# Performance work log

Hardware: AMD Instinct MI355X
Metric: run time of the kernel (lower is better)

## Reference

```python
import jax, jax.numpy as jnp
import numpy as np

B, N, D, H = 4, 8192, 1024, 8
HD = D // H  # 128
EPS = 1e-5


def setup_inputs() -> dict:
    key = jax.random.key(0)
    k1, k2, k3 = jax.random.split(key, 3)
    x = jax.random.normal(k1, (B, N, D), dtype=jnp.float32)
    mask = jax.random.randint(k2, (B, 1, N), 0, 2).astype(jnp.bool_)
    # nn.Linear(dim, 3*dim, bias=False): weight [3D, D]; store as [D, 3D] for x @ w
    w_qkv = jax.random.normal(k3, (D, 3 * D), dtype=jnp.float32) / np.sqrt(D)
    gamma = jnp.ones((D,), dtype=jnp.float32)
    beta = jnp.zeros((D,), dtype=jnp.float32)
    return {"x": x, "mask": mask, "w_qkv": w_qkv, "gamma": gamma, "beta": beta}


def _layernorm(x, gamma, beta):
    mu = jnp.mean(x, axis=-1, keepdims=True)
    var = jnp.mean(jnp.square(x - mu), axis=-1, keepdims=True)
    return (x - mu) * jax.lax.rsqrt(var + EPS) * gamma + beta


def reference(x, mask, w_qkv, gamma, beta):
    xn = _layernorm(x, gamma, beta)                       # [B,N,D]
    qkv = xn @ w_qkv                                      # [B,N,3D]
    q, k, v = jnp.split(qkv, 3, axis=-1)
    # 'b n (h d) -> b h n d'
    def to_heads(t):
        return t.reshape(B, N, H, HD).transpose(0, 2, 1, 3)
    q, k, v = to_heads(q), to_heads(k), to_heads(v)       # [B,H,N,HD]
    q = jax.nn.sigmoid(q)
    k = jnp.tanh(k)
    k = jnp.where(mask[..., None], 0.0, k)                # masked_fill -> 0
    kv = jnp.einsum('bhnd,bhne->bhde', k, v)              # k^T @ v, [B,H,HD,HD]
    out = jnp.einsum('bhnd,bhde->bhne', q, kv)            # [B,H,N,HD]
    out = out.transpose(0, 2, 1, 3).reshape(B, N, D)      # 'b h n d -> b n (h d)'
    return out  # output_layer='None' -> Identity
```

## Files before the change

kernel.cpp:

```cpp
#include <hip/hip_runtime.h>

#define EPS 1e-5f
#define B_ 4
#define N_ 8192
#define D_ 1024
#define H_ 8
#define HD_ 128
#define M_TOT 32768
#define NQKV 3072

typedef __bf16 bf16x8 __attribute__((ext_vector_type(8)));
typedef float f32x4 __attribute__((ext_vector_type(4)));

__device__ __forceinline__ float bf2f(unsigned short u) {
    unsigned int v = ((unsigned int)u) << 16;
    return __uint_as_float(v);
}
__device__ __forceinline__ unsigned short f2bf(float f) {
    unsigned int u = __float_as_uint(f);
    u += 0x7fffu + ((u >> 16) & 1u);
    return (unsigned short)(u >> 16);
}

__device__ __forceinline__ float fast_sigmoid(float v) {
    return __builtin_amdgcn_rcpf(1.0f + __expf(-v));
}
__device__ __forceinline__ float fast_tanh(float v) {
    return 1.0f - 2.0f * __builtin_amdgcn_rcpf(1.0f + __expf(2.0f * v));
}

__device__ __forceinline__ void gl_lds16(const void* g, void* l) {
    __builtin_amdgcn_global_load_lds(
        (const __attribute__((address_space(1))) unsigned int*)g,
        (__attribute__((address_space(3))) unsigned int*)l, 16, 0, 0);
}

__global__ __launch_bounds__(256) void ln_kernel(const float* __restrict__ x,
                                                 const float* __restrict__ gamma,
                                                 const float* __restrict__ beta,
                                                 unsigned short* __restrict__ xn) {
    const int row = blockIdx.x;
    const int t = threadIdx.x;
    const float* xr = x + (size_t)row * D_;
    float4 xv = ((const float4*)xr)[t];
    float s = xv.x + xv.y + xv.z + xv.w;
    float s2 = xv.x * xv.x + xv.y * xv.y + xv.z * xv.z + xv.w * xv.w;
    for (int off = 32; off > 0; off >>= 1) {
        s += __shfl_down(s, off);
        s2 += __shfl_down(s2, off);
    }
    __shared__ float red[8];
    if ((t & 63) == 0) { red[t >> 6] = s; red[4 + (t >> 6)] = s2; }
    __syncthreads();
    float ts = red[0] + red[1] + red[2] + red[3];
    float ts2 = red[4] + red[5] + red[6] + red[7];
    float mu = ts * (1.0f / D_);
    float var = ts2 * (1.0f / D_) - mu * mu;
    float rs = rsqrtf(var + EPS);
    float4 g = ((const float4*)gamma)[t];
    float4 bt = ((const float4*)beta)[t];
    ushort4 o;
    o.x = f2bf((xv.x - mu) * rs * g.x + bt.x);
    o.y = f2bf((xv.y - mu) * rs * g.y + bt.y);
    o.z = f2bf((xv.z - mu) * rs * g.z + bt.z);
    o.w = f2bf((xv.w - mu) * rs * g.w + bt.w);
    ((ushort4*)(xn + (size_t)row * D_))[t] = o;
}

__global__ __launch_bounds__(256) void wt_kernel(const float* __restrict__ w,
                                                 unsigned short* __restrict__ wT) {
    __shared__ float tile[64][65];
    const int n0 = blockIdx.x * 64;
    const int k0 = blockIdx.y * 64;
    const int t = threadIdx.x;
    const int tx = t & 63, ty = t >> 6;
    #pragma unroll
    for (int i = 0; i < 16; i++) {
        int r = i * 4 + ty;
        tile[r][tx] = w[(size_t)(k0 + r) * NQKV + n0 + tx];
    }
    __syncthreads();
    #pragma unroll
    for (int i = 0; i < 16; i++) {
        int r = i * 4 + ty;
        wT[(size_t)(n0 + r) * D_ + k0 + tx] = f2bf(tile[tx][r]);
    }
}

#define CT_STRIDE 136
__global__ __launch_bounds__(256, 3) void qkv_gemm(const unsigned short* __restrict__ xn,
                                                   const unsigned short* __restrict__ wT,
                                                   const int* __restrict__ mask,
                                                   unsigned short* __restrict__ qws,
                                                   unsigned short* __restrict__ kT,
                                                   unsigned short* __restrict__ vT) {
    __shared__ unsigned short ShB[128 * CT_STRIDE];
    const int t = threadIdx.x;
    const int w = t >> 6, l = t & 63;
    const int quad = l >> 4, ln16 = l & 15;
    const int m0 = blockIdx.y * 128;
    const int n0 = blockIdx.x * 128;
    const int wm = (w >> 1) * 64, wn = (w & 1) * 64;

    f32x4 acc[4][4] = {};

    const unsigned short* aG = xn + (size_t)(m0 + w * 16 + (l >> 2)) * D_ + (l & 3) * 8;
    const unsigned short* bG = wT + (size_t)(n0 + w * 16 + (l >> 2)) * D_ + (l & 3) * 8;
    char* SB = (char*)ShB;

    for (int k0 = 0; k0 < 1024; k0 += 64) {
        #pragma unroll
        for (int s = 0; s < 2; s++) {
            gl_lds16(aG + k0 + s * 32,            SB + s * 8192 + w * 1024);
            gl_lds16(aG + 64 * D_ + k0 + s * 32,  SB + s * 8192 + 4096 + w * 1024);
            gl_lds16(bG + k0 + s * 32,            SB + 16384 + s * 8192 + w * 1024);
            gl_lds16(bG + 64 * D_ + k0 + s * 32,  SB + 16384 + s * 8192 + 4096 + w * 1024);
        }
        __syncthreads();
        #pragma unroll
        for (int s = 0; s < 2; s++) {
            const char* A0 = SB + s * 8192;
            const char* B0 = SB + 16384 + s * 8192;
            bf16x8 af[4], bfr[4];
            #pragma unroll
            for (int mi = 0; mi < 4; mi++)
                af[mi] = *(const bf16x8*)(A0 + (wm + mi * 16 + ln16) * 64 + quad * 16);
            #pragma unroll
            for (int ni = 0; ni < 4; ni++)
                bfr[ni] = *(const bf16x8*)(B0 + (wn + ni * 16 + ln16) * 64 + quad * 16);
            #pragma unroll
            for (int mi = 0; mi < 4; mi++)
                #pragma unroll
                for (int ni = 0; ni < 4; ni++)
                    acc[mi][ni] = __builtin_amdgcn_mfma_f32_16x16x32_bf16(af[mi], bfr[ni],
                                                                          acc[mi][ni], 0, 0, 0);
        }
        __syncthreads();
    }

    const int region = n0 >> 10;
    const int cbase = n0 & 1023;
    if (region == 0) {
        #pragma unroll
        for (int mi = 0; mi < 4; mi++) {
            #pragma unroll
            for (int r = 0; r < 4; r++) {
                int gm = m0 + wm + mi * 16 + quad * 4 + r;
                #pragma unroll
                for (int ni = 0; ni < 4; ni++) {
                    int cc = cbase + wn + ni * 16 + ln16;
                    qws[(size_t)gm * D_ + cc] = f2bf(fast_sigmoid(acc[mi][ni][r]));
                }
            }
        }
    } else {
        #pragma unroll
        for (int mi = 0; mi < 4; mi++) {
            int tok0 = wm + mi * 16 + quad * 4;
            int mk0 = 0, mk1 = 0, mk2 = 0, mk3 = 0;
            if (region == 1) {
                mk0 = mask[m0 + tok0];
                mk1 = mask[m0 + tok0 + 1];
                mk2 = mask[m0 + tok0 + 2];
                mk3 = mask[m0 + tok0 + 3];
            }
            #pragma unroll
            for (int ni = 0; ni < 4; ni++) {
                int fl = wn + ni * 16 + ln16;
                float v0 = acc[mi][ni][0], v1 = acc[mi][ni][1];
                float v2 = acc[mi][ni][2], v3 = acc[mi][ni][3];
                if (region == 1) {
                    v0 = mk0 ? 0.0f : fast_tanh(v0);
                    v1 = mk1 ? 0.0f : fast_tanh(v1);
                    v2 = mk2 ? 0.0f : fast_tanh(v2);
                    v3 = mk3 ? 0.0f : fast_tanh(v3);
                }
                ushort4 pk;
                pk.x = f2bf(v0); pk.y = f2bf(v1); pk.z = f2bf(v2); pk.w = f2bf(v3);
                *(ushort4*)&ShB[fl * CT_STRIDE + tok0] = pk;
            }
        }
        __syncthreads();
        unsigned short* dstT = (region == 1) ? kT : vT;
        const int h = cbase >> 7;
        const int b = m0 >> 13;
        const int ntok0 = m0 & 8191;
        #pragma unroll
        for (int p = 0; p < 8; p++) {
            int fl = p * 16 + (t >> 4);
            int tok = (t & 15) * 8;
            uint4 u = *(const uint4*)&ShB[fl * CT_STRIDE + tok];
            *(uint4*)(dstT + ((size_t)(b * 8 + h) * 128 + fl) * 8192 + ntok0 + tok) = u;
        }
    }
}

__global__ __launch_bounds__(256) void kv_mfma(const unsigned short* __restrict__ kT,
                                               const unsigned short* __restrict__ vT,
                                               float* __restrict__ kv) {
    __shared__ unsigned short As[128 * 32];
    __shared__ unsigned short Bs[128 * 32];
    const int t = threadIdx.x;
    const int w = t >> 6, l = t & 63;
    const int quad = l >> 4, ln16 = l & 15;
    const int bh = blockIdx.y;
    const int kc0 = blockIdx.x * 512;
    const int wm = (w >> 1) * 64, wn = (w & 1) * 64;

    f32x4 acc[4][4] = {};

    const size_t base = (size_t)bh * 128 * 8192;
    const unsigned short* aG = kT + base + (size_t)(w * 16 + (l >> 2)) * 8192
                               + (l & 3) * 8 + kc0;
    const unsigned short* bG = vT + base + (size_t)(w * 16 + (l >> 2)) * 8192
                               + (l & 3) * 8 + kc0;
    char* AsB = (char*)As;
    char* BsB = (char*)Bs;
    char* aL0 = AsB + w * 1024;
    char* aL1 = AsB + 4096 + w * 1024;
    char* bL0 = BsB + w * 1024;
    char* bL1 = BsB + 4096 + w * 1024;

    for (int kk = 0; kk < 512; kk += 32) {
        gl_lds16(aG + kk, aL0);
        gl_lds16(aG + 64 * 8192 + kk, aL1);
        gl_lds16(bG + kk, bL0);
        gl_lds16(bG + 64 * 8192 + kk, bL1);
        __syncthreads();
        bf16x8 af[4], bfr[4];
        #pragma unroll
        for (int mi = 0; mi < 4; mi++)
            af[mi] = *(const bf16x8*)(AsB + (wm + mi * 16 + ln16) * 64 + quad * 16);
        #pragma unroll
        for (int ni = 0; ni < 4; ni++)
            bfr[ni] = *(const bf16x8*)(BsB + (wn + ni * 16 + ln16) * 64 + quad * 16);
        #pragma unroll
        for (int mi = 0; mi < 4; mi++)
            #pragma unroll
            for (int ni = 0; ni < 4; ni++)
                acc[mi][ni] = __builtin_amdgcn_mfma_f32_16x16x32_bf16(af[mi], bfr[ni],
                                                                      acc[mi][ni], 0, 0, 0);
        __syncthreads();
    }

    float* dst = kv + (size_t)bh * (HD_ * HD_);
    #pragma unroll
    for (int mi = 0; mi < 4; mi++) {
        #pragma unroll
        for (int r = 0; r < 4; r++) {
            int d = wm + mi * 16 + quad * 4 + r;
            #pragma unroll
            for (int ni = 0; ni < 4; ni++) {
                int e = wn + ni * 16 + ln16;
                atomicAdd(&dst[d * HD_ + e], acc[mi][ni][r]);
            }
        }
    }
}

__global__ __launch_bounds__(256) void kvcvt(const float* __restrict__ kv,
                                             unsigned short* __restrict__ kvTb) {
    __shared__ float tile[32][132];
    const int bh = blockIdx.x;
    const int c = blockIdx.y;
    const int t = threadIdx.x;
    {
        int r = t >> 3, cc = (t & 7) * 16;
        const float* src = kv + ((size_t)bh * 128 + c * 32 + r) * 128 + cc;
        #pragma unroll
        for (int q4 = 0; q4 < 4; q4++)
            *(float4*)&tile[r][cc + q4 * 4] = *(const float4*)(src + q4 * 4);
    }
    __syncthreads();
    {
        int e = t >> 1, dh = t & 1;
        ushort4 o[4];
        #pragma unroll
        for (int q4 = 0; q4 < 4; q4++) {
            o[q4].x = f2bf(tile[dh * 16 + q4 * 4 + 0][e]);
            o[q4].y = f2bf(tile[dh * 16 + q4 * 4 + 1][e]);
            o[q4].z = f2bf(tile[dh * 16 + q4 * 4 + 2][e]);
            o[q4].w = f2bf(tile[dh * 16 + q4 * 4 + 3][e]);
        }
        unsigned short* dst = kvTb + (size_t)bh * 16384 + e * 128 + c * 32 + dh * 16;
        #pragma unroll
        for (int q4 = 0; q4 < 4; q4++)
            ((ushort4*)dst)[q4] = o[q4];
    }
}

__global__ __launch_bounds__(256) void out_mfma(const unsigned short* __restrict__ qws,
                                                const unsigned short* __restrict__ kvTb,
                                                float* __restrict__ out) {
    __shared__ unsigned short As[128 * 32];
    __shared__ unsigned short Bs[128 * 32];
    const int t = threadIdx.x;
    const int w = t >> 6, l = t & 63;
    const int quad = l >> 4, ln16 = l & 15;
    const int m0 = blockIdx.x * 128;
    const int h = blockIdx.y;
    const int b = m0 >> 13;
    const int bh = b * 8 + h;
    const int wm = (w >> 1) * 64, wn = (w & 1) * 64;

    f32x4 acc[4][4] = {};

    const unsigned short* aG = qws + (size_t)(m0 + w * 16 + (l >> 2)) * D_
                               + h * HD_ + (l & 3) * 8;
    const unsigned short* bG = kvTb + (size_t)bh * 16384
                               + (size_t)(w * 16 + (l >> 2)) * 128 + (l & 3) * 8;
    char* AsB = (char*)As;
    char* BsB = (char*)Bs;

    for (int kk = 0; kk < 128; kk += 32) {
        gl_lds16(aG + kk, AsB + w * 1024);
        gl_lds16(aG + 64 * D_ + kk, AsB + 4096 + w * 1024);
        gl_lds16(bG + kk, BsB + w * 1024);
        gl_lds16(bG + 64 * 128 + kk, BsB + 4096 + w * 1024);
        __syncthreads();
        bf16x8 af[4], bfr[4];
        #pragma unroll
        for (int mi = 0; mi < 4; mi++)
            af[mi] = *(const bf16x8*)(AsB + (wm + mi * 16 + ln16) * 64 + quad * 16);
        #pragma unroll
        for (int ni = 0; ni < 4; ni++)
            bfr[ni] = *(const bf16x8*)(BsB + (wn + ni * 16 + ln16) * 64 + quad * 16);
        #pragma unroll
        for (int mi = 0; mi < 4; mi++)
            #pragma unroll
            for (int ni = 0; ni < 4; ni++)
                acc[mi][ni] = __builtin_amdgcn_mfma_f32_16x16x32_bf16(af[mi], bfr[ni],
                                                                      acc[mi][ni], 0, 0, 0);
        __syncthreads();
    }

    #pragma unroll
    for (int mi = 0; mi < 4; mi++) {
        #pragma unroll
        for (int r = 0; r < 4; r++) {
            int gm = m0 + wm + mi * 16 + quad * 4 + r;
            #pragma unroll
            for (int ni = 0; ni < 4; ni++) {
                int e = wn + ni * 16 + ln16;
                out[(size_t)gm * D_ + h * HD_ + e] = acc[mi][ni][r];
            }
        }
    }
}

extern "C" void kernel_launch(void* const* d_in, const int* in_sizes, int n_in,
                              void* d_out, int out_size, void* d_ws, size_t ws_size,
                              hipStream_t stream) {
    const float* x     = (const float*)d_in[0];
    const int*   mask  = (const int*)d_in[1];
    const float* w     = (const float*)d_in[2];
    const float* gamma = (const float*)d_in[3];
    const float* beta  = (const float*)d_in[4];
    float* out = (float*)d_out;
    char* ws = (char*)d_ws;

    unsigned short* xn  = (unsigned short*)(ws + 0);
    unsigned short* wT  = (unsigned short*)(ws + 67108864ull);
    unsigned short* qws = (unsigned short*)(ws + 73400320ull);
    unsigned short* kT  = (unsigned short*)(ws + 140509184ull);
    unsigned short* vT  = (unsigned short*)(ws + 207618048ull);
    float* kv           = (float*)(ws + 274726912ull);
    unsigned short* kvTb = (unsigned short*)(ws + 276824064ull);

    hipMemsetAsync(kv, 0, 32 * HD_ * HD_ * sizeof(float), stream);
    hipLaunchKernelGGL(ln_kernel, dim3(M_TOT), dim3(256), 0, stream, x, gamma, beta, xn);
    hipLaunchKernelGGL(wt_kernel, dim3(48, 16), dim3(256), 0, stream, w, wT);
    hipLaunchKernelGGL(qkv_gemm, dim3(NQKV / 128, M_TOT / 128), dim3(256), 0, stream,
                       xn, wT, mask, qws, kT, vT);
    hipLaunchKernelGGL(kv_mfma, dim3(16, 32), dim3(256), 0, stream, kT, vT, kv);
    hipLaunchKernelGGL(kvcvt, dim3(32, 4), dim3(256), 0, stream, kv, kvTb);
    hipLaunchKernelGGL(out_mfma, dim3(M_TOT / 128, 8), dim3(256), 0, stream,
                       qws, kvTb, out);
}
```

Measured before the change: 544.6 us.

## Use one-wave LayerNorm, swizzled LDS tiles, and partial-sum KV reduction without atomics

LayerNorm now runs one 64-thread wave per row and reduces with shuffles, which drops the shared-memory reduction and its barrier. kv_mfma loads 64-wide K chunks into XOR-swizzled LDS and writes per-chunk partial KV sums to a buffer in place of float atomics. kvcvt then sums those 16 partials, which also removes the memset. out_mfma loads the full 128-wide K tile into 64 KB of swizzled LDS once, with a single barrier. The costs are more LDS per block, which may limit occupancy, and extra partial-buffer traffic; the partial buffer reuses the xn workspace region.

```diff
diff --git a/kernel.cpp b/kernel.cpp
--- a/kernel.cpp
+++ b/kernel.cpp
@@ -35,36 +35,45 @@
         (__attribute__((address_space(3))) unsigned int*)l, 16, 0, 0);
 }
 
-__global__ __launch_bounds__(256) void ln_kernel(const float* __restrict__ x,
-                                                 const float* __restrict__ gamma,
-                                                 const float* __restrict__ beta,
-                                                 unsigned short* __restrict__ xn) {
+__global__ __launch_bounds__(64) void ln_kernel(const float* __restrict__ x,
+                                                const float* __restrict__ gamma,
+                                                const float* __restrict__ beta,
+                                                unsigned short* __restrict__ xn) {
     const int row = blockIdx.x;
     const int t = threadIdx.x;
     const float* xr = x + (size_t)row * D_;
-    float4 xv = ((const float4*)xr)[t];
-    float s = xv.x + xv.y + xv.z + xv.w;
-    float s2 = xv.x * xv.x + xv.y * xv.y + xv.z * xv.z + xv.w * xv.w;
+    float4 xv[4];
+    #pragma unroll
+    for (int i = 0; i < 4; i++) xv[i] = ((const float4*)xr)[i * 64 + t];
+    float s = 0.0f, s2 = 0.0f;
+    #pragma unroll
+    for (int i = 0; i < 4; i++) {
+        s  += xv[i].x + xv[i].y + xv[i].z + xv[i].w;
+        s2 += xv[i].x * xv[i].x + xv[i].y * xv[i].y
+            + xv[i].z * xv[i].z + xv[i].w * xv[i].w;
+    }
+    #pragma unroll
     for (int off = 32; off > 0; off >>= 1) {
-        s += __shfl_down(s, off);
+        s  += __shfl_down(s, off);
         s2 += __shfl_down(s2, off);
     }
-    __shared__ float red[8];
-    if ((t & 63) == 0) { red[t >> 6] = s; red[4 + (t >> 6)] = s2; }
-    __syncthreads();
-    float ts = red[0] + red[1] + red[2] + red[3];
-    float ts2 = red[4] + red[5] + red[6] + red[7];
-    float mu = ts * (1.0f / D_);
-    float var = ts2 * (1.0f / D_) - mu * mu;
-    float rs = rsqrtf(var + EPS);
-    float4 g = ((const float4*)gamma)[t];
-    float4 bt = ((const float4*)beta)[t];
-    ushort4 o;
-    o.x = f2bf((xv.x - mu) * rs * g.x + bt.x);
-    o.y = f2bf((xv.y - mu) * rs * g.y + bt.y);
-    o.z = f2bf((xv.z - mu) * rs * g.z + bt.z);
-    o.w = f2bf((xv.w - mu) * rs * g.w + bt.w);
-    ((ushort4*)(xn + (size_t)row * D_))[t] = o;
+    s = __shfl(s, 0);
+    s2 = __shfl(s2, 0);
+    const float mu = s * (1.0f / D_);
+    const float var = s2 * (1.0f / D_) - mu * mu;
+    const float rs = rsqrtf(var + EPS);
+    unsigned short* xo = xn + (size_t)row * D_;
+    #pragma unroll
+    for (int i = 0; i < 4; i++) {
+        float4 g  = ((const float4*)gamma)[i * 64 + t];
+        float4 bt = ((const float4*)beta)[i * 64 + t];
+        ushort4 o;
+        o.x = f2bf((xv[i].x - mu) * rs * g.x + bt.x);
+        o.y = f2bf((xv[i].y - mu) * rs * g.y + bt.y);
+        o.z = f2bf((xv[i].z - mu) * rs * g.z + bt.z);
+        o.w = f2bf((xv[i].w - mu) * rs * g.w + bt.w);
+        ((ushort4*)xo)[i * 64 + t] = o;
+    }
 }
 
 __global__ __launch_bounds__(256) void wt_kernel(const float* __restrict__ w,
@@ -197,9 +206,10 @@
 
 __global__ __launch_bounds__(256) void kv_mfma(const unsigned short* __restrict__ kT,
                                                const unsigned short* __restrict__ vT,
-                                               float* __restrict__ kv) {
-    __shared__ unsigned short As[128 * 32];
-    __shared__ unsigned short Bs[128 * 32];
+                                               float* __restrict__ kvp) {
+    __shared__ __align__(16) char smem[32768];
+    char* AsB = smem;
+    char* BsB = smem + 16384;
     const int t = threadIdx.x;
     const int w = t >> 6, l = t & 63;
     const int quad = l >> 4, ln16 = l & 15;
@@ -210,40 +220,46 @@
     f32x4 acc[4][4] = {};
 
     const size_t base = (size_t)bh * 128 * 8192;
-    const unsigned short* aG = kT + base + (size_t)(w * 16 + (l >> 2)) * 8192
-                               + (l & 3) * 8 + kc0;
-    const unsigned short* bG = vT + base + (size_t)(w * 16 + (l >> 2)) * 8192
-                               + (l & 3) * 8 + kc0;
-    char* AsB = (char*)As;
-    char* BsB = (char*)Bs;
-    char* aL0 = AsB + w * 1024;
-    char* aL1 = AsB + 4096 + w * 1024;
-    char* bL0 = BsB + w * 1024;
-    char* bL1 = BsB + 4096 + w * 1024;
-
-    for (int kk = 0; kk < 512; kk += 32) {
-        gl_lds16(aG + kk, aL0);
-        gl_lds16(aG + 64 * 8192 + kk, aL1);
-        gl_lds16(bG + kk, bL0);
-        gl_lds16(bG + 64 * 8192 + kk, bL1);
+    const int gsw = (l & 7) ^ (l >> 3);
+    const unsigned short* aG = kT + base + (size_t)(w * 8 + (l >> 3)) * 8192 + kc0 + gsw * 8;
+    const unsigned short* bG = vT + base + (size_t)(w * 8 + (l >> 3)) * 8192 + kc0 + gsw * 8;
+    const int r7 = ln16 & 7;
+    const int kb0 = ((quad ^ r7) << 4);
+    const int kb1 = (((4 | quad) ^ r7) << 4);
+
+    for (int kk = 0; kk < 512; kk += 64) {
+        #pragma unroll
+        for (int c = 0; c < 4; c++) {
+            gl_lds16(aG + (size_t)(c * 32) * 8192 + kk, AsB + c * 4096 + w * 1024);
+            gl_lds16(bG + (size_t)(c * 32) * 8192 + kk, BsB + c * 4096 + w * 1024);
+        }
         __syncthreads();
-        bf16x8 af[4], bfr[4];
+        bf16x8 af[4][2], bfr[4][2];
+        #pragma unroll
+        for (int mi = 0; mi < 4; mi++) {
+            const char* rp = AsB + (wm + mi * 16 + ln16) * 128;
+            af[mi][0] = *(const bf16x8*)(rp + kb0);
+            af[mi][1] = *(const bf16x8*)(rp + kb1);
+        }
+        #pragma unroll
+        for (int ni = 0; ni < 4; ni++) {
+            const char* rp = BsB + (wn + ni * 16 + ln16) * 128;
+            bfr[ni][0] = *(const bf16x8*)(rp + kb0);
+            bfr[ni][1] = *(const bf16x8*)(rp + kb1);
+        }
         #pragma unroll
         for (int mi = 0; mi < 4; mi++)
-            af[mi] = *(const bf16x8*)(AsB + (wm + mi * 16 + ln16) * 64 + quad * 16);
-        #pragma unroll
-        for (int ni = 0; ni < 4; ni++)
-            bfr[ni] = *(const bf16x8*)(BsB + (wn + ni * 16 + ln16) * 64 + quad * 16);
-        #pragma unroll
-        for (int mi = 0; mi < 4; mi++)
-            #pragma unroll
-            for (int ni = 0; ni < 4; ni++)
-                acc[mi][ni] = __builtin_amdgcn_mfma_f32_16x16x32_bf16(af[mi], bfr[ni],
+            #pragma unroll
+            for (int ni = 0; ni < 4; ni++) {
+                acc[mi][ni] = __builtin_amdgcn_mfma_f32_16x16x32_bf16(af[mi][0], bfr[ni][0],
                                                                       acc[mi][ni], 0, 0, 0);
+                acc[mi][ni] = __builtin_amdgcn_mfma_f32_16x16x32_bf16(af[mi][1], bfr[ni][1],
+                                                                      acc[mi][ni], 0, 0, 0);
+            }
         __syncthreads();
     }
 
-    float* dst = kv + (size_t)bh * (HD_ * HD_);
+    float* dst = kvp + ((size_t)blockIdx.x * 32 + bh) * (HD_ * HD_);
     #pragma unroll
     for (int mi = 0; mi < 4; mi++) {
         #pragma unroll
@@ -252,13 +268,13 @@
             #pragma unroll
             for (int ni = 0; ni < 4; ni++) {
                 int e = wn + ni * 16 + ln16;
-                atomicAdd(&dst[d * HD_ + e], acc[mi][ni][r]);
-            }
-        }
-    }
-}
-
-__global__ __launch_bounds__(256) void kvcvt(const float* __restrict__ kv,
+                dst[d * HD_ + e] = acc[mi][ni][r];
+            }
+        }
+    }
+}
+
+__global__ __launch_bounds__(256) void kvcvt(const float* __restrict__ kvp,
                                              unsigned short* __restrict__ kvTb) {
     __shared__ float tile[32][132];
     const int bh = blockIdx.x;
@@ -266,10 +282,17 @@
     const int t = threadIdx.x;
     {
         int r = t >> 3, cc = (t & 7) * 16;
-        const float* src = kv + ((size_t)bh * 128 + c * 32 + r) * 128 + cc;
+        f32x4 s[4] = {};
+        for (int p = 0; p < 16; p++) {
+            const float* src = kvp + ((size_t)p * 32 + bh) * (HD_ * HD_)
+                               + (size_t)(c * 32 + r) * 128 + cc;
+            #pragma unroll
+            for (int q4 = 0; q4 < 4; q4++)
+                s[q4] += *(const f32x4*)(src + q4 * 4);
+        }
         #pragma unroll
         for (int q4 = 0; q4 < 4; q4++)
-            *(float4*)&tile[r][cc + q4 * 4] = *(const float4*)(src + q4 * 4);
+            *(f32x4*)&tile[r][cc + q4 * 4] = s[q4];
     }
     __syncthreads();
     {
@@ -292,8 +315,9 @@
 __global__ __launch_bounds__(256) void out_mfma(const unsigned short* __restrict__ qws,
                                                 const unsigned short* __restrict__ kvTb,
                                                 float* __restrict__ out) {
-    __shared__ unsigned short As[128 * 32];
-    __shared__ unsigned short Bs[128 * 32];
+    __shared__ __align__(16) char smem[65536];
+    char* AsB = smem;
+    char* BsB = smem + 32768;
     const int t = threadIdx.x;
     const int w = t >> 6, l = t & 63;
     const int quad = l >> 4, ln16 = l & 15;
@@ -303,35 +327,36 @@
     const int bh = b * 8 + h;
     const int wm = (w >> 1) * 64, wn = (w & 1) * 64;
 
+    const int gsw = (l & 15) ^ (w * 4 + (l >> 4));
+    const unsigned short* aG = qws + (size_t)(m0 + w * 4 + (l >> 4)) * D_
+                               + h * HD_ + gsw * 8;
+    const unsigned short* bG = kvTb + (size_t)bh * 16384
+                               + (size_t)(w * 4 + (l >> 4)) * 128 + gsw * 8;
+    #pragma unroll
+    for (int c = 0; c < 8; c++) {
+        gl_lds16(aG + (size_t)(c * 16) * D_, AsB + c * 4096 + w * 1024);
+        gl_lds16(bG + (c * 16) * 128,        BsB + c * 4096 + w * 1024);
+    }
+    __syncthreads();
+
     f32x4 acc[4][4] = {};
-
-    const unsigned short* aG = qws + (size_t)(m0 + w * 16 + (l >> 2)) * D_
-                               + h * HD_ + (l & 3) * 8;
-    const unsigned short* bG = kvTb + (size_t)bh * 16384
-                               + (size_t)(w * 16 + (l >> 2)) * 128 + (l & 3) * 8;
-    char* AsB = (char*)As;
-    char* BsB = (char*)Bs;
-
-    for (int kk = 0; kk < 128; kk += 32) {
-        gl_lds16(aG + kk, AsB + w * 1024);
-        gl_lds16(aG + 64 * D_ + kk, AsB + 4096 + w * 1024);
-        gl_lds16(bG + kk, BsB + w * 1024);
-        gl_lds16(bG + 64 * 128 + kk, BsB + 4096 + w * 1024);
-        __syncthreads();
+    #pragma unroll
+    for (int ks = 0; ks < 4; ks++) {
         bf16x8 af[4], bfr[4];
         #pragma unroll
         for (int mi = 0; mi < 4; mi++)
-            af[mi] = *(const bf16x8*)(AsB + (wm + mi * 16 + ln16) * 64 + quad * 16);
+            af[mi] = *(const bf16x8*)(AsB + (wm + mi * 16 + ln16) * 256
+                                      + ((((ks * 4) + quad) ^ ln16) << 4));
         #pragma unroll
         for (int ni = 0; ni < 4; ni++)
-            bfr[ni] = *(const bf16x8*)(BsB + (wn + ni * 16 + ln16) * 64 + quad * 16);
+            bfr[ni] = *(const bf16x8*)(BsB + (wn + ni * 16 + ln16) * 256
+                                       + ((((ks * 4) + quad) ^ ln16) << 4));
         #pragma unroll
         for (int mi = 0; mi < 4; mi++)
             #pragma unroll
             for (int ni = 0; ni < 4; ni++)
                 acc[mi][ni] = __builtin_amdgcn_mfma_f32_16x16x32_bf16(af[mi], bfr[ni],
                                                                       acc[mi][ni], 0, 0, 0);
-        __syncthreads();
     }
 
     #pragma unroll
@@ -364,16 +389,15 @@
     unsigned short* qws = (unsigned short*)(ws + 73400320ull);
     unsigned short* kT  = (unsigned short*)(ws + 140509184ull);
     unsigned short* vT  = (unsigned short*)(ws + 207618048ull);
-    float* kv           = (float*)(ws + 274726912ull);
-    unsigned short* kvTb = (unsigned short*)(ws + 276824064ull);
-
-    hipMemsetAsync(kv, 0, 32 * HD_ * HD_ * sizeof(float), stream);
-    hipLaunchKernelGGL(ln_kernel, dim3(M_TOT), dim3(256), 0, stream, x, gamma, beta, xn);
+    unsigned short* kvTb = (unsigned short*)(ws + 274726912ull);
+    float* kvp = (float*)(ws + 0);
+
+    hipLaunchKernelGGL(ln_kernel, dim3(M_TOT), dim3(64), 0, stream, x, gamma, beta, xn);
     hipLaunchKernelGGL(wt_kernel, dim3(48, 16), dim3(256), 0, stream, w, wT);
     hipLaunchKernelGGL(qkv_gemm, dim3(NQKV / 128, M_TOT / 128), dim3(256), 0, stream,
                        xn, wT, mask, qws, kT, vT);
-    hipLaunchKernelGGL(kv_mfma, dim3(16, 32), dim3(256), 0, stream, kT, vT, kv);
-    hipLaunchKernelGGL(kvcvt, dim3(32, 4), dim3(256), 0, stream, kv, kvTb);
+    hipLaunchKernelGGL(kv_mfma, dim3(16, 32), dim3(256), 0, stream, kT, vT, kvp);
+    hipLaunchKernelGGL(kvcvt, dim3(32, 4), dim3(256), 0, stream, kvp, kvTb);
     hipLaunchKernelGGL(out_mfma, dim3(M_TOT / 128, 8), dim3(256), 0, stream,
                        qws, kvTb, out);
 }
```

After: 524.1 us. 3.8% less time.
